# Optimization experiments

Hardware: AMD Instinct MI355X
Metric: run time of the kernel (lower is better)

Reference implementation:

```python
import jax, jax.numpy as jnp
import numpy as np

B, INPUT, MEM, CELL, HEADS, K = 32, 512, 32768, 64, 1, 16
VIS = K + 1  # visible_size = sparse_reads + 1


def setup_inputs() -> dict:
    key = jax.random.key(0)
    ks = jax.random.split(key, 8)
    n = lambda k, s: jax.random.normal(k, s, jnp.float32)
    scale = 0.05  # small init so tanh/sigmoid stay in useful range
    return {
        "xi": n(ks[0], (B, INPUT)),
        "memory": n(ks[1], (B, MEM, CELL)),
        "least_used_mem": jax.random.randint(ks[2], (B, 1), 0, MEM),
        "W_rq": n(ks[3], (HEADS * CELL, INPUT)) * scale,
        "b_rq": jnp.zeros((HEADS * CELL,), jnp.float32),
        "W_wv": n(ks[4], (CELL, INPUT)) * scale,
        "b_wv": jnp.zeros((CELL,), jnp.float32),
        "W_ig": n(ks[5], (VIS, INPUT)) * scale,
        "b_ig": jnp.zeros((VIS,), jnp.float32),
        "W_wg": n(ks[6], (1, INPUT)) * scale,
        "b_wg": jnp.zeros((1,), jnp.float32),
    }


def reference(xi, memory, least_used_mem, W_rq, b_rq, W_wv, b_wv, W_ig, b_ig, W_wg, b_wg):
    b = xi.shape[0]
    # interface transforms (independent_linears=True path)
    read_query = jnp.tanh(xi @ W_rq.T + b_rq).reshape(b, HEADS, CELL)
    write_vector = jnp.tanh(xi @ W_wv.T + b_wv).reshape(b, 1, CELL)
    interpolation_gate = jax.nn.sigmoid(xi @ W_ig.T + b_ig)          # [b, VIS]
    write_gate = jax.nn.sigmoid(xi @ W_wg.T + b_wg)                  # [b, 1]

    # kNN search over memory (torch.topk fallback path of read_from_sparse_memory)
    sims = jnp.einsum("bhc,bmc->bhm", read_query, memory)            # [b, H, MEM]
    _, idx = jax.lax.top_k(sims, K)                                  # [b, H, K]
    read_positions = jnp.concatenate([idx.reshape(b, -1), least_used_mem], axis=1)  # [b, VIS]

    # gather visible memory cells
    visible_memory = jnp.take_along_axis(memory, read_positions[:, :, None], axis=1)  # [b, VIS, CELL]

    # attention over visible cells
    rw = jax.nn.softmax(jnp.einsum("bhc,bvc->bhv", read_query, visible_memory), axis=2)  # [b, H, VIS]
    read_vectors = jnp.einsum("bhv,bvc->bhc", rw, visible_memory)    # [b, H, CELL]
    rw_flat = rw.sum(axis=1)                                         # [b, VIS]

    # scatter read weights into full memory-sized vector (torch scatter_ = set)
    read_weights = jnp.zeros((b, MEM), xi.dtype).at[
        jnp.arange(b)[:, None], read_positions
    ].set(rw_flat)                                                   # [b, MEM]

    return read_vectors, read_weights, visible_memory, write_vector, interpolation_gate, write_gate
```

## Files before the change

kernel.cpp:

```cpp
#include <hip/hip_runtime.h>
#include <cstdint>
#include <cstddef>
#include <cfloat>
#include <cmath>

#define NB    32
#define NIN   512
#define NMEM  32768
#define NCELL 64
#define NVIS  17
#define NK    16
#define NBLK  32
#define RPB   (NMEM / NBLK)

#define OFF_RV  0
#define OFF_RW  2048
#define OFF_VIS 1050624
#define OFF_WV  1085440
#define OFF_IG  1087488
#define OFF_WG  1088032

#define SCR_RQ  0
#define SCR_CV  64
#define SCR_CI  576
#define SCR_STRIDE_WS 1088

__global__ __launch_bounds__(256) void kA(
    const float* __restrict__ xi,
    const float* __restrict__ Wrq, const float* __restrict__ brq,
    const float* __restrict__ Wwv, const float* __restrict__ bwv,
    const float* __restrict__ Wig, const float* __restrict__ big,
    const float* __restrict__ Wwg, const float* __restrict__ bwg,
    float* __restrict__ scr_base, int scr_stride,
    float* __restrict__ out)
{
    int b = blockIdx.x;
    int tid = threadIdx.x;
    float* rq_scr = scr_base + (size_t)b * scr_stride + SCR_RQ;
    __shared__ float sxi[NIN];
    for (int i = tid; i < NIN; i += 256)
        sxi[i] = xi[(size_t)b * NIN + i];
    __syncthreads();
    int g = tid >> 3, sub = tid & 7;
    int row = blockIdx.y * 32 + g;
    if (row < 146) {
        const float* W; float bias; int kind, r;
        if (row < 64)       { r = row;       W = Wrq + (size_t)r * NIN; bias = brq[r]; kind = 0; }
        else if (row < 128) { r = row - 64;  W = Wwv + (size_t)r * NIN; bias = bwv[r]; kind = 1; }
        else if (row < 145) { r = row - 128; W = Wig + (size_t)r * NIN; bias = big[r]; kind = 2; }
        else                { r = 0;         W = Wwg;                   bias = bwg[0]; kind = 3; }
        float acc = 0.f;
        const float* wp = W   + sub * 64;
        const float* xp = sxi + sub * 64;
        for (int j = 0; j < 64; ++j)
            acc = fmaf(wp[j], xp[j], acc);
        acc += __shfl_xor(acc, 1);
        acc += __shfl_xor(acc, 2);
        acc += __shfl_xor(acc, 4);
        if (sub == 0) {
            float x = acc + bias;
            if (kind == 0)      rq_scr[r] = tanhf(x);
            else if (kind == 1) out[OFF_WV + b * NCELL + r] = tanhf(x);
            else if (kind == 2) out[OFF_IG + b * NVIS + r]  = 1.f / (1.f + expf(-x));
            else                out[OFF_WG + b]             = 1.f / (1.f + expf(-x));
        }
    }
}

__global__ __launch_bounds__(256) void kB(
    const float* __restrict__ mem,
    float* __restrict__ scr_base, int scr_stride, int kb_zero,
    float* __restrict__ out)
{
    int b   = blockIdx.y;
    int blk = blockIdx.x;
    int tid = threadIdx.x;
    int w = tid >> 6, lane = tid & 63;
    int sub = lane & 7;
    float* scr = scr_base + (size_t)b * scr_stride;
    __shared__ float ssim[4][256];
    __shared__ float wcv[64];
    __shared__ int   wci[64];

    if (kb_zero) {
        float4 z; z.x = z.y = z.z = z.w = 0.f;
        ((float4*)(out + OFF_RW + (size_t)b * NMEM + blk * RPB))[tid] = z;
    }

    float rqv[8];
    for (int e = 0; e < 8; ++e) rqv[e] = scr[SCR_RQ + sub * 8 + e];

    const float* mb = mem + (size_t)b * NMEM * NCELL + (size_t)(blk * RPB + w * 256) * NCELL;

    for (int it = 0; it < 32; ++it) {
        int lr = it * 8 + (lane >> 3);
        const float* rp = mb + (size_t)lr * NCELL + sub * 8;
        float4 a = *(const float4*)rp;
        float4 d = *(const float4*)(rp + 4);
        float acc = 0.f;
        acc = fmaf(a.x, rqv[0], acc); acc = fmaf(a.y, rqv[1], acc);
        acc = fmaf(a.z, rqv[2], acc); acc = fmaf(a.w, rqv[3], acc);
        acc = fmaf(d.x, rqv[4], acc); acc = fmaf(d.y, rqv[5], acc);
        acc = fmaf(d.z, rqv[6], acc); acc = fmaf(d.w, rqv[7], acc);
        acc += __shfl_xor(acc, 1);
        acc += __shfl_xor(acc, 2);
        acc += __shfl_xor(acc, 4);
        if (sub == 0) ssim[w][lr] = acc;
    }
    __syncthreads();

    int gbase = blk * RPB + w * 256;
    float v[4]; int gi[4];
    for (int j = 0; j < 4; ++j) {
        v[j]  = ssim[w][lane * 4 + j];
        gi[j] = gbase + lane * 4 + j;
    }
    for (int r = 0; r < NK; ++r) {
        float bv = v[0]; int bi = gi[0];
        for (int j = 1; j < 4; ++j)
            if (v[j] > bv || (v[j] == bv && gi[j] < bi)) { bv = v[j]; bi = gi[j]; }
        for (int off = 32; off >= 1; off >>= 1) {
            float ov = __shfl_xor(bv, off); int oi = __shfl_xor(bi, off);
            if (ov > bv || (ov == bv && oi < bi)) { bv = ov; bi = oi; }
        }
        for (int j = 0; j < 4; ++j)
            if (gi[j] == bi) { v[j] = -FLT_MAX; gi[j] = 0x7fffffff; }
        if (lane == 0) { wcv[w * 16 + r] = bv; wci[w * 16 + r] = bi; }
    }
    __syncthreads();

    if (w == 0) {
        float mv2 = wcv[lane]; int mi2 = wci[lane];
        float* ovp = scr + SCR_CV + blk * NK;
        int*   oip = (int*)(scr + SCR_CI) + blk * NK;
        for (int r = 0; r < NK; ++r) {
            float bv = mv2; int bi = mi2;
            for (int off = 32; off >= 1; off >>= 1) {
                float ov = __shfl_xor(bv, off); int oi = __shfl_xor(bi, off);
                if (ov > bv || (ov == bv && oi < bi)) { bv = ov; bi = oi; }
            }
            if (mi2 == bi) { mv2 = -FLT_MAX; mi2 = 0x7fffffff; }
            if (lane == 0) { ovp[r] = bv; oip[r] = bi; }
        }
    }
}

__global__ __launch_bounds__(256) void kC(
    const float* __restrict__ mem, const int* __restrict__ lum,
    const float* __restrict__ scr_base, int scr_stride, int kc_zero,
    float* __restrict__ out)
{
    int b = blockIdx.x;
    int tid = threadIdx.x;
    int w = tid >> 6, lane = tid & 63;
    float* rwrow = out + OFF_RW + (size_t)b * NMEM;
    const float* scr = scr_base + (size_t)b * scr_stride;
    __shared__ float lv[NBLK * NK];
    __shared__ int   li[NBLK * NK];
    __shared__ int   pos_s[NVIS];
    __shared__ float sc_s[NVIS];
    __shared__ float rw_s[NVIS];
    __shared__ float pacc[4][NCELL];

    for (int j = 0; j < 2; ++j) {
        int e = tid * 2 + j;
        lv[e] = scr[SCR_CV + e];
        li[e] = ((const int*)(scr + SCR_CI))[e];
    }
    __syncthreads();

    if (w == 0) {
        float v[8]; int gi[8];
        for (int j = 0; j < 8; ++j) { v[j] = lv[lane * 8 + j]; gi[j] = li[lane * 8 + j]; }
        for (int r = 0; r < NK; ++r) {
            float bv = v[0]; int bi = gi[0];
            for (int j = 1; j < 8; ++j)
                if (v[j] > bv || (v[j] == bv && gi[j] < bi)) { bv = v[j]; bi = gi[j]; }
            for (int off = 32; off >= 1; off >>= 1) {
                float ov = __shfl_xor(bv, off); int oi = __shfl_xor(bi, off);
                if (ov > bv || (ov == bv && oi < bi)) { bv = ov; bi = oi; }
            }
            for (int j = 0; j < 8; ++j)
                if (gi[j] == bi) { v[j] = -FLT_MAX; gi[j] = 0x7fffffff; }
            if (lane == 0) { pos_s[r] = bi & (NMEM - 1); sc_s[r] = bv; }
        }
        int p16 = lum[b] & (NMEM - 1);
        float x = mem[((size_t)b * NMEM + p16) * NCELL + lane] * scr[SCR_RQ + lane];
        for (int off = 32; off >= 1; off >>= 1) x += __shfl_xor(x, off);
        if (lane == 0) { pos_s[NK] = p16; sc_s[NK] = x; }
    }
    __syncthreads();

    if (w == 0) {
        float sc = (lane < NVIS) ? sc_s[lane] : -FLT_MAX;
        float mx = sc;
        for (int off = 32; off >= 1; off >>= 1) mx = fmaxf(mx, __shfl_xor(mx, off));
        float e = (lane < NVIS) ? expf(sc - mx) : 0.f;
        float sum = e;
        for (int off = 32; off >= 1; off >>= 1) sum += __shfl_xor(sum, off);
        if (lane < NVIS) rw_s[lane] = e / sum;
    }
    __syncthreads();

    if (kc_zero) {
        for (int it = 0; it < 128; ++it)
            rwrow[it * 256 + tid] = 0.f;
    }

    float acc = 0.f;
    for (int vv = w; vv < NVIS; vv += 4) {
        int p = pos_s[vv] & (NMEM - 1);
        float hv = mem[((size_t)b * NMEM + p) * NCELL + lane];
        out[OFF_VIS + ((size_t)b * NVIS + vv) * NCELL + lane] = hv;
        acc = fmaf(rw_s[vv], hv, acc);
    }
    pacc[w][lane] = acc;
    __syncthreads();

    if (tid < NCELL) {
        float s = pacc[0][tid] + pacc[1][tid] + pacc[2][tid] + pacc[3][tid];
        out[OFF_RV + b * NCELL + tid] = s;
    }
    if (tid < NVIS) {
        int p = pos_s[tid] & (NMEM - 1);
        bool dup = (tid < NK) && (p == pos_s[NK]);
        if (!dup) rwrow[p] = rw_s[tid];
    }
}

extern "C" void kernel_launch(void* const* d_in, const int* in_sizes, int n_in,
                              void* d_out, int out_size, void* d_ws, size_t ws_size,
                              hipStream_t stream)
{
    const float* xi  = (const float*)d_in[0];
    const float* mem = (const float*)d_in[1];
    const int*   lum = (const int*)d_in[2];
    const float* Wrq = (const float*)d_in[3];
    const float* brq = (const float*)d_in[4];
    const float* Wwv = (const float*)d_in[5];
    const float* bwv = (const float*)d_in[6];
    const float* Wig = (const float*)d_in[7];
    const float* big = (const float*)d_in[8];
    const float* Wwg = (const float*)d_in[9];
    const float* bwg = (const float*)d_in[10];
    float* out = (float*)d_out;

    bool use_ws = (d_ws != nullptr) && (ws_size >= (size_t)NB * SCR_STRIDE_WS * 4);
    float* scrb = use_ws ? (float*)d_ws : out + OFF_RW;
    int    scrs = use_ws ? SCR_STRIDE_WS : NMEM;
    int    kb_zero = use_ws ? 1 : 0;
    int    kc_zero = use_ws ? 0 : 1;

    kA<<<dim3(NB, 5), dim3(256), 0, stream>>>(xi, Wrq, brq, Wwv, bwv, Wig, big,
                                              Wwg, bwg, scrb, scrs, out);
    kB<<<dim3(NBLK, NB), dim3(256), 0, stream>>>(mem, scrb, scrs, kb_zero, out);
    kC<<<dim3(NB), dim3(256), 0, stream>>>(mem, lum, scrb, scrs, kc_zero, out);
}
```

Before: 91.10 us.

## Double similarity-scan blocks per batch and widen per-lane row loads

Splits each batch's memory scan across 64 blocks instead of 32, so the grid fills more compute units on the bandwidth-bound similarity pass. The inner loop now uses 16 lanes per row with four independent rows in flight per iteration, which gives more outstanding loads per wave. In exchange the final merge kernel must select the top 16 from 1024 candidates instead of 512, so its serial single-wave selection takes longer, and the scratch layout grows to match.

Measured after the change: 129.7 us. 42.4% more time.

```diff
diff --git a/kernel.cpp b/kernel.cpp
--- a/kernel.cpp
+++ b/kernel.cpp
@@ -10,8 +10,9 @@
 #define NCELL 64
 #define NVIS  17
 #define NK    16
-#define NBLK  32
+#define NBLK  64
 #define RPB   (NMEM / NBLK)
+#define NCAND (NBLK * NK)
 
 #define OFF_RV  0
 #define OFF_RW  2048
@@ -22,8 +23,8 @@
 
 #define SCR_RQ  0
 #define SCR_CV  64
-#define SCR_CI  576
-#define SCR_STRIDE_WS 1088
+#define SCR_CI  1088
+#define SCR_STRIDE_WS 2112
 
 __global__ __launch_bounds__(256) void kA(
     const float* __restrict__ xi,
@@ -76,54 +77,75 @@
     int blk = blockIdx.x;
     int tid = threadIdx.x;
     int w = tid >> 6, lane = tid & 63;
-    int sub = lane & 7;
+    int sub16 = lane & 15, grp4 = lane >> 4;
     float* scr = scr_base + (size_t)b * scr_stride;
-    __shared__ float ssim[4][256];
+    __shared__ float ssim[4][128];
     __shared__ float wcv[64];
     __shared__ int   wci[64];
 
     if (kb_zero) {
-        float4 z; z.x = z.y = z.z = z.w = 0.f;
-        ((float4*)(out + OFF_RW + (size_t)b * NMEM + blk * RPB))[tid] = z;
-    }
-
-    float rqv[8];
-    for (int e = 0; e < 8; ++e) rqv[e] = scr[SCR_RQ + sub * 8 + e];
-
-    const float* mb = mem + (size_t)b * NMEM * NCELL + (size_t)(blk * RPB + w * 256) * NCELL;
-
-    for (int it = 0; it < 32; ++it) {
-        int lr = it * 8 + (lane >> 3);
-        const float* rp = mb + (size_t)lr * NCELL + sub * 8;
-        float4 a = *(const float4*)rp;
-        float4 d = *(const float4*)(rp + 4);
-        float acc = 0.f;
-        acc = fmaf(a.x, rqv[0], acc); acc = fmaf(a.y, rqv[1], acc);
-        acc = fmaf(a.z, rqv[2], acc); acc = fmaf(a.w, rqv[3], acc);
-        acc = fmaf(d.x, rqv[4], acc); acc = fmaf(d.y, rqv[5], acc);
-        acc = fmaf(d.z, rqv[6], acc); acc = fmaf(d.w, rqv[7], acc);
-        acc += __shfl_xor(acc, 1);
-        acc += __shfl_xor(acc, 2);
-        acc += __shfl_xor(acc, 4);
-        if (sub == 0) ssim[w][lr] = acc;
-    }
-    __syncthreads();
-
-    int gbase = blk * RPB + w * 256;
-    float v[4]; int gi[4];
-    for (int j = 0; j < 4; ++j) {
-        v[j]  = ssim[w][lane * 4 + j];
-        gi[j] = gbase + lane * 4 + j;
+        float2 z; z.x = z.y = 0.f;
+        ((float2*)(out + OFF_RW + (size_t)b * NMEM + blk * RPB))[tid] = z;
+    }
+
+    float rq4[4];
+    for (int e = 0; e < 4; ++e) rq4[e] = scr[SCR_RQ + sub16 * 4 + e];
+
+    const float* mb = mem + (size_t)b * NMEM * NCELL + (size_t)(blk * RPB + w * 128) * NCELL;
+
+    for (int it = 0; it < 8; ++it) {
+        int rbase = it * 16;
+        const float* p0 = mb + (size_t)(rbase +  0 + grp4) * NCELL + sub16 * 4;
+        const float* p1 = mb + (size_t)(rbase +  4 + grp4) * NCELL + sub16 * 4;
+        const float* p2 = mb + (size_t)(rbase +  8 + grp4) * NCELL + sub16 * 4;
+        const float* p3 = mb + (size_t)(rbase + 12 + grp4) * NCELL + sub16 * 4;
+        float4 x0 = *(const float4*)p0;
+        float4 x1 = *(const float4*)p1;
+        float4 x2 = *(const float4*)p2;
+        float4 x3 = *(const float4*)p3;
+
+        float s0 = 0.f, s1 = 0.f, s2 = 0.f, s3 = 0.f;
+        s0 = fmaf(x0.x, rq4[0], s0); s0 = fmaf(x0.y, rq4[1], s0);
+        s0 = fmaf(x0.z, rq4[2], s0); s0 = fmaf(x0.w, rq4[3], s0);
+        s1 = fmaf(x1.x, rq4[0], s1); s1 = fmaf(x1.y, rq4[1], s1);
+        s1 = fmaf(x1.z, rq4[2], s1); s1 = fmaf(x1.w, rq4[3], s1);
+        s2 = fmaf(x2.x, rq4[0], s2); s2 = fmaf(x2.y, rq4[1], s2);
+        s2 = fmaf(x2.z, rq4[2], s2); s2 = fmaf(x2.w, rq4[3], s2);
+        s3 = fmaf(x3.x, rq4[0], s3); s3 = fmaf(x3.y, rq4[1], s3);
+        s3 = fmaf(x3.z, rq4[2], s3); s3 = fmaf(x3.w, rq4[3], s3);
+
+        s0 += __shfl_xor(s0, 1); s0 += __shfl_xor(s0, 2);
+        s0 += __shfl_xor(s0, 4); s0 += __shfl_xor(s0, 8);
+        s1 += __shfl_xor(s1, 1); s1 += __shfl_xor(s1, 2);
+        s1 += __shfl_xor(s1, 4); s1 += __shfl_xor(s1, 8);
+        s2 += __shfl_xor(s2, 1); s2 += __shfl_xor(s2, 2);
+        s2 += __shfl_xor(s2, 4); s2 += __shfl_xor(s2, 8);
+        s3 += __shfl_xor(s3, 1); s3 += __shfl_xor(s3, 2);
+        s3 += __shfl_xor(s3, 4); s3 += __shfl_xor(s3, 8);
+
+        if (sub16 == 0) {
+            ssim[w][rbase +  0 + grp4] = s0;
+            ssim[w][rbase +  4 + grp4] = s1;
+            ssim[w][rbase +  8 + grp4] = s2;
+            ssim[w][rbase + 12 + grp4] = s3;
+        }
+    }
+    __syncthreads();
+
+    int gbase = blk * RPB + w * 128;
+    float v[2]; int gi[2];
+    for (int j = 0; j < 2; ++j) {
+        v[j]  = ssim[w][lane * 2 + j];
+        gi[j] = gbase + lane * 2 + j;
     }
     for (int r = 0; r < NK; ++r) {
         float bv = v[0]; int bi = gi[0];
-        for (int j = 1; j < 4; ++j)
-            if (v[j] > bv || (v[j] == bv && gi[j] < bi)) { bv = v[j]; bi = gi[j]; }
+        if (v[1] > bv || (v[1] == bv && gi[1] < bi)) { bv = v[1]; bi = gi[1]; }
         for (int off = 32; off >= 1; off >>= 1) {
             float ov = __shfl_xor(bv, off); int oi = __shfl_xor(bi, off);
             if (ov > bv || (ov == bv && oi < bi)) { bv = ov; bi = oi; }
         }
-        for (int j = 0; j < 4; ++j)
+        for (int j = 0; j < 2; ++j)
             if (gi[j] == bi) { v[j] = -FLT_MAX; gi[j] = 0x7fffffff; }
         if (lane == 0) { wcv[w * 16 + r] = bv; wci[w * 16 + r] = bi; }
     }
@@ -155,32 +177,32 @@
     int w = tid >> 6, lane = tid & 63;
     float* rwrow = out + OFF_RW + (size_t)b * NMEM;
     const float* scr = scr_base + (size_t)b * scr_stride;
-    __shared__ float lv[NBLK * NK];
-    __shared__ int   li[NBLK * NK];
+    __shared__ float lv[NCAND];
+    __shared__ int   li[NCAND];
     __shared__ int   pos_s[NVIS];
     __shared__ float sc_s[NVIS];
     __shared__ float rw_s[NVIS];
     __shared__ float pacc[4][NCELL];
 
-    for (int j = 0; j < 2; ++j) {
-        int e = tid * 2 + j;
+    for (int j = 0; j < 4; ++j) {
+        int e = tid * 4 + j;
         lv[e] = scr[SCR_CV + e];
         li[e] = ((const int*)(scr + SCR_CI))[e];
     }
     __syncthreads();
 
     if (w == 0) {
-        float v[8]; int gi[8];
-        for (int j = 0; j < 8; ++j) { v[j] = lv[lane * 8 + j]; gi[j] = li[lane * 8 + j]; }
+        float v[16]; int gi[16];
+        for (int j = 0; j < 16; ++j) { v[j] = lv[lane * 16 + j]; gi[j] = li[lane * 16 + j]; }
         for (int r = 0; r < NK; ++r) {
             float bv = v[0]; int bi = gi[0];
-            for (int j = 1; j < 8; ++j)
+            for (int j = 1; j < 16; ++j)
                 if (v[j] > bv || (v[j] == bv && gi[j] < bi)) { bv = v[j]; bi = gi[j]; }
             for (int off = 32; off >= 1; off >>= 1) {
                 float ov = __shfl_xor(bv, off); int oi = __shfl_xor(bi, off);
                 if (ov > bv || (ov == bv && oi < bi)) { bv = ov; bi = oi; }
             }
-            for (int j = 0; j < 8; ++j)
+            for (int j = 0; j < 16; ++j)
                 if (gi[j] == bi) { v[j] = -FLT_MAX; gi[j] = 0x7fffffff; }
             if (lane == 0) { pos_s[r] = bi & (NMEM - 1); sc_s[r] = bv; }
         }
```
